# Kernel optimization log

Hardware: AMD Instinct MI355X
Metric: run time of the kernel (lower is better)

Reference implementation:

```python
import jax, jax.numpy as jnp
import numpy as np

H = 128
N = 20000
E = 640000

def _lin_params(key, fan_in, fan_out, bias=True):
    k1, k2 = jax.random.split(key)
    bound = 1.0 / np.sqrt(fan_in)
    W = jax.random.uniform(k1, (fan_in, fan_out), jnp.float32, -bound, bound)
    if bias:
        b = jax.random.uniform(k2, (fan_out,), jnp.float32, -bound, bound)
        return W, b
    return W, None

def setup_inputs() -> dict:
    key = jax.random.key(0)
    ks = jax.random.split(key, 10)
    h = jax.random.normal(ks[0], (N, H), jnp.float32)
    pos = jax.random.normal(ks[1], (N, 3), jnp.float32)
    edge_index = jax.random.randint(ks[2], (2, E), 0, N, jnp.int64)
    eW1, eb1 = _lin_params(ks[3], 2 * H + 1, H)
    eW2, eb2 = _lin_params(ks[4], H, H)
    cW1, cb1 = _lin_params(ks[5], H, H)
    cW2, _ = _lin_params(ks[6], H, 1, bias=False)
    nW1, nb1 = _lin_params(ks[7], 2 * H, H)
    nW2, nb2 = _lin_params(ks[8], H, H)
    return {"h": h, "pos": pos, "edge_index": edge_index,
            "eW1": eW1, "eb1": eb1, "eW2": eW2, "eb2": eb2,
            "cW1": cW1, "cb1": cb1, "cW2": cW2,
            "nW1": nW1, "nb1": nb1, "nW2": nW2, "nb2": nb2}

def reference(h, pos, edge_index, eW1, eb1, eW2, eb2, cW1, cb1, cW2, nW1, nb1, nW2, nb2):
    row, col = edge_index[0], edge_index[1]
    n = h.shape[0]
    # per-edge geometry
    coord_diff = pos[row] - pos[col]                      # [E, 3]
    sq_dists = jnp.sum(coord_diff ** 2, axis=-1, keepdims=True)  # [E, 1]
    # edge MLP: Linear -> SiLU -> Linear -> SiLU
    edge_inputs = jnp.concatenate([h[row], h[col], sq_dists], axis=-1)  # [E, 2H+1]
    m_ij = jax.nn.silu(jax.nn.silu(edge_inputs @ eW1 + eb1) @ eW2 + eb2)  # [E, H]
    # coord MLP: Linear -> SiLU -> Linear(no bias) -> scalar weight per edge
    coord_weights = jax.nn.silu(m_ij @ cW1 + cb1) @ cW2   # [E, 1]
    norm_coord_diff = coord_diff / jnp.sqrt(sq_dists + 1e-8)
    pos_updates_ij = norm_coord_diff * coord_weights      # [E, 3]
    # scatter-mean over target nodes (zero where a node has no edges)
    pos_sum = jax.ops.segment_sum(pos_updates_ij, row, num_segments=n)
    cnt = jax.ops.segment_sum(jnp.ones((row.shape[0], 1), h.dtype), row, num_segments=n)
    pos_out = pos + pos_sum / jnp.maximum(cnt, 1.0)
    # scatter-add messages, then node MLP with residual
    m_i = jax.ops.segment_sum(m_ij, row, num_segments=n)  # [N, H]
    node_inputs = jnp.concatenate([h, m_i], axis=-1)      # [N, 2H]
    h_out = h + (jax.nn.silu(node_inputs @ nW1 + nb1) @ nW2 + nb2)
    return h_out, pos_out
```

## Files before the change

### kernel.cpp

```cpp
#include <hip/hip_runtime.h>
#include <hip/hip_bf16.h>
#include <cstdint>

#define H 128
#define NNODES 20000
#define NEDGES 640000
#define TILE 64
#define SCAN_BLOCKS 20

typedef unsigned short ushort_t;
typedef __attribute__((ext_vector_type(8))) short short8;
typedef __attribute__((ext_vector_type(4))) float floatx4;
typedef __attribute__((ext_vector_type(2))) float floatx2;

__device__ __forceinline__ ushort_t f2bf(float f){
  uint32_t u = __builtin_bit_cast(uint32_t, f);
  u += 0x7fffu + ((u >> 16) & 1u);
  return (ushort_t)(u >> 16);
}
__device__ __forceinline__ float bf2f(ushort_t s){
  uint32_t u = ((uint32_t)s) << 16;
  return __builtin_bit_cast(float, u);
}
__device__ __forceinline__ uint32_t pk2bf(float lo, float hi){
  __hip_bfloat162 h2 = __float22bfloat162_rn(make_float2(lo, hi));
  uint32_t u;
  __builtin_memcpy(&u, &h2, 4);
  return u;
}
__device__ __forceinline__ floatx2 bfpair2(uint32_t u){
  floatx2 r;
  r.x = __builtin_bit_cast(float, u << 16);
  r.y = __builtin_bit_cast(float, u & 0xffff0000u);
  return r;
}
__device__ __forceinline__ float silu_f(float x){
  float e = __builtin_amdgcn_exp2f(-1.44269504089f * x);
  return x * __builtin_amdgcn_rcpf(1.f + e);
}

__global__ void setup_kernel(const float* __restrict__ eW1, const float* __restrict__ eW2,
                             const float* __restrict__ cW1, const float* __restrict__ nW1,
                             const float* __restrict__ nW2, const int* __restrict__ ei,
                             ushort_t* __restrict__ eW1t, ushort_t* __restrict__ eW2t,
                             ushort_t* __restrict__ cW1t, ushort_t* __restrict__ nW1t,
                             ushort_t* __restrict__ nW2t, uint32_t* __restrict__ w256b,
                             int* __restrict__ hist, float4* __restrict__ zbase){
  int idx = blockIdx.x * 256 + threadIdx.x;
  if (idx < 32768){
    int n = idx >> 8, k = idx & 255;
    eW1t[idx] = f2bf(eW1[k * H + n]);
  } else if (idx < 49152){
    int j = idx - 32768; int n = j >> 7, k = j & 127;
    eW2t[j] = f2bf(eW2[k * H + n]);
  } else if (idx < 65536){
    int j = idx - 49152; int n = j >> 7, k = j & 127;
    cW1t[j] = f2bf(cW1[k * H + n]);
  } else if (idx < 98304){
    int j = idx - 65536; int n = j >> 8, k = j & 255;
    nW1t[j] = f2bf(nW1[k * H + n]);
  } else if (idx < 114688){
    int j = idx - 98304; int n = j >> 7, k = j & 127;
    nW2t[j] = f2bf(nW2[k * H + n]);
  } else if (idx < 114752){
    int j = idx - 114688;
    w256b[j] = pk2bf(eW1[256 * H + 2*j], eW1[256 * H + 2*j + 1]);
  } else if (idx < 754752){
    int j = idx - 114752;
    atomicAdd(&hist[ei[j]], 1);
  } else {
    int j = idx - 754752;
    if (j < 655000) zbase[j] = make_float4(0.f, 0.f, 0.f, 0.f);
  }
}

__global__ void pq_kernel(const float* __restrict__ h, const ushort_t* __restrict__ eW1t,
                          const ushort_t* __restrict__ nW1t, const float* __restrict__ eb1,
                          ushort_t* __restrict__ Pb, ushort_t* __restrict__ Qb,
                          ushort_t* __restrict__ Rb){
  const int t = threadIdx.x;
  const int lane = t & 63, q = lane >> 4, ln = lane & 15;
  const int nb = (t >> 6) * 32;
  const int c0 = nb + 2 * ln;
  const int base = blockIdx.x * 64;

  floatx4 accP[4][2], accQ[4][2], accR[4][2];
  #pragma unroll
  for (int mt = 0; mt < 4; mt++)
    #pragma unroll
    for (int nt = 0; nt < 2; nt++){
      accP[mt][nt] = (floatx4)0.f; accQ[mt][nt] = (floatx4)0.f; accR[mt][nt] = (floatx4)0.f;
    }

  #pragma unroll
  for (int ks = 0; ks < 4; ks++){
    short8 a[4];
    #pragma unroll
    for (int mt = 0; mt < 4; mt++){
      int node = base + mt*16 + ln;
      if (node >= NNODES) node = NNODES - 1;
      const float* hp = h + (size_t)node * H + ks*32 + q*8;
      float4 v0 = *(const float4*)hp;
      float4 v1 = *(const float4*)(hp + 4);
      uint32_t tw[4];
      tw[0] = pk2bf(v0.x, v0.y); tw[1] = pk2bf(v0.z, v0.w);
      tw[2] = pk2bf(v1.x, v1.y); tw[3] = pk2bf(v1.z, v1.w);
      __builtin_memcpy(&a[mt], tw, 16);
    }
    short8 bP[2], bQ[2], bR[2];
    #pragma unroll
    for (int nt = 0; nt < 2; nt++){
      bP[nt] = *(const short8*)(eW1t + (size_t)(c0 + nt) * 256 + ks*32 + q*8);
      bQ[nt] = *(const short8*)(eW1t + (size_t)(c0 + nt) * 256 + 128 + ks*32 + q*8);
      bR[nt] = *(const short8*)(nW1t + (size_t)(c0 + nt) * 256 + ks*32 + q*8);
    }
    #pragma unroll
    for (int mt = 0; mt < 4; mt++)
      #pragma unroll
      for (int nt = 0; nt < 2; nt++){
        accP[mt][nt] = __builtin_amdgcn_mfma_f32_16x16x32_bf16(a[mt], bP[nt], accP[mt][nt], 0, 0, 0);
        accQ[mt][nt] = __builtin_amdgcn_mfma_f32_16x16x32_bf16(a[mt], bQ[nt], accQ[mt][nt], 0, 0, 0);
        accR[mt][nt] = __builtin_amdgcn_mfma_f32_16x16x32_bf16(a[mt], bR[nt], accR[mt][nt], 0, 0, 0);
      }
  }
  float2 e1 = *(const float2*)(eb1 + c0);
  #pragma unroll
  for (int mt = 0; mt < 4; mt++)
    #pragma unroll
    for (int r = 0; r < 4; r++){
      int node = base + mt*16 + q*4 + r;
      if (node < NNODES){
        *(uint32_t*)(Pb + (size_t)node * H + c0) = pk2bf(accP[mt][0][r] + e1.x, accP[mt][1][r] + e1.y);
        *(uint32_t*)(Qb + (size_t)node * H + c0) = pk2bf(accQ[mt][0][r], accQ[mt][1][r]);
        *(uint32_t*)(Rb + (size_t)node * H + c0) = pk2bf(accR[mt][0][r], accR[mt][1][r]);
      }
    }
}

__global__ void scanA_kernel(const int* __restrict__ hist, int* __restrict__ head,
                             int* __restrict__ totals){
  __shared__ int s[1024];
  const int t = threadIdx.x;
  const int idx = blockIdx.x * 1024 + t;
  int v = (idx < NNODES) ? hist[idx] : 0;
  s[t] = v;
  __syncthreads();
  for (int off = 1; off < 1024; off <<= 1){
    int tmp = (t >= off) ? s[t - off] : 0;
    __syncthreads();
    s[t] += tmp;
    __syncthreads();
  }
  if (idx < NNODES) head[idx] = s[t] - v;
  if (t == 1023) totals[blockIdx.x] = s[t];
}

__global__ void scanC_kernel(const int* __restrict__ totals, int* __restrict__ head){
  __shared__ int off_s;
  if (threadIdx.x == 0){
    int a = 0;
    for (int i = 0; i < (int)blockIdx.x; i++) a += totals[i];
    off_s = a;
  }
  __syncthreads();
  int idx = blockIdx.x * 1024 + threadIdx.x;
  if (idx < NNODES) head[idx] += off_s;
}

__global__ void scatter_kernel(const int* __restrict__ ei, int* __restrict__ head,
                               int2* __restrict__ spair){
  int idx = blockIdx.x * 256 + threadIdx.x;
  if (idx < NEDGES){
    int r = ei[idx], c = ei[NEDGES + idx];
    int p = atomicAdd(&head[r], 1);
    spair[p] = make_int2(r, c);
  }
}

__global__ __launch_bounds__(256, 8) void edge_kernel(
    const ushort_t* __restrict__ Pb, const ushort_t* __restrict__ Qb,
    const float* __restrict__ pos, const int2* __restrict__ spair,
    const uint32_t* __restrict__ w256b,
    const float* __restrict__ eb2, const float* __restrict__ cb1,
    const float* __restrict__ cW2,
    const ushort_t* __restrict__ eW2t, const ushort_t* __restrict__ cW1t,
    float* __restrict__ m_i, float* __restrict__ pos_sum)
{
  __shared__ __align__(16) ushort_t buf[TILE * 136];
  __shared__ int   row_l[TILE];
  __shared__ float sq_l[TILE];
  __shared__ float dx_l[TILE], dy_l[TILE], dz_l[TILE], w_l[TILE];

  const int t = threadIdx.x;
  const int base = blockIdx.x * TILE;
  const int lane = t & 63, q = lane >> 4, ln = lane & 15;
  const int nb = (t >> 6) * 32;
  const int c0 = nb + 2 * ln;

  {
    const int i = t >> 2, p = t & 3;
    int2 rc = spair[base + i];
    float ax = pos[rc.x*3+0] - pos[rc.y*3+0];
    float ay = pos[rc.x*3+1] - pos[rc.y*3+1];
    float az = pos[rc.x*3+2] - pos[rc.y*3+2];
    float sq = ax*ax + ay*ay + az*az;
    if (p == 0){
      row_l[i] = rc.x; sq_l[i] = sq;
      dx_l[i] = ax; dy_l[i] = ay; dz_l[i] = az;
      w_l[i] = 0.f;
    }
    floatx2 sq2; sq2.x = sq; sq2.y = sq;
    const uint4* Pp = (const uint4*)(Pb + (size_t)rc.x * H + p*32);
    const uint4* Qp = (const uint4*)(Qb + (size_t)rc.y * H + p*32);
    const uint4* Wp = (const uint4*)(w256b + p*16);
    ushort_t* dst = buf + i * 136 + p*32;
    #pragma unroll
    for (int j = 0; j < 4; j++){
      uint4 pv = Pp[j], qv = Qp[j], wv = Wp[j];
      uint32_t pvv[4] = {pv.x, pv.y, pv.z, pv.w};
      uint32_t qvv[4] = {qv.x, qv.y, qv.z, qv.w};
      uint32_t wvv[4] = {wv.x, wv.y, wv.z, wv.w};
      uint32_t outv[4];
      #pragma unroll
      for (int e = 0; e < 4; e++){
        floatx2 f = bfpair2(pvv[e]) + bfpair2(qvv[e]) + sq2 * bfpair2(wvv[e]);
        outv[e] = pk2bf(silu_f(f.x), silu_f(f.y));
      }
      uint4 out; __builtin_memcpy(&out, outv, 16);
      *(uint4*)(dst + j*8) = out;
    }
  }
  __syncthreads();

  floatx4 acc[4][2];

  #pragma unroll
  for (int mt = 0; mt < 4; mt++)
    #pragma unroll
    for (int nt = 0; nt < 2; nt++) acc[mt][nt] = (floatx4)0.f;
  #pragma unroll
  for (int ks = 0; ks < 4; ks++){
    short8 a[4], b[2];
    #pragma unroll
    for (int mt = 0; mt < 4; mt++)
      a[mt] = *(const short8*)(buf + (mt*16 + ln) * 136 + ks*32 + q*8);
    #pragma unroll
    for (int nt = 0; nt < 2; nt++)
      b[nt] = *(const short8*)(eW2t + (size_t)(c0 + nt) * 128 + ks*32 + q*8);
    #pragma unroll
    for (int mt = 0; mt < 4; mt++)
      #pragma unroll
      for (int nt = 0; nt < 2; nt++)
        acc[mt][nt] = __builtin_amdgcn_mfma_f32_16x16x32_bf16(a[mt], b[nt], acc[mt][nt], 0, 0, 0);
  }
  __syncthreads();
  {
    float2 e2 = *(const float2*)(eb2 + c0);
    #pragma unroll
    for (int mt = 0; mt < 4; mt++)
      #pragma unroll
      for (int r = 0; r < 4; r++){
        int m = mt*16 + q*4 + r;
        float f0 = silu_f(acc[mt][0][r] + e2.x);
        float f1 = silu_f(acc[mt][1][r] + e2.y);
        *(uint32_t*)(buf + m * 136 + c0) = pk2bf(f0, f1);
      }
  }
  __syncthreads();

  #pragma unroll
  for (int mt = 0; mt < 4; mt++)
    #pragma unroll
    for (int nt = 0; nt < 2; nt++) acc[mt][nt] = (floatx4)0.f;
  #pragma unroll
  for (int ks = 0; ks < 4; ks++){
    short8 a[4], b[2];
    #pragma unroll
    for (int mt = 0; mt < 4; mt++)
      a[mt] = *(const short8*)(buf + (mt*16 + ln) * 136 + ks*32 + q*8);
    #pragma unroll
    for (int nt = 0; nt < 2; nt++)
      b[nt] = *(const short8*)(cW1t + (size_t)(c0 + nt) * 128 + ks*32 + q*8);
    #pragma unroll
    for (int mt = 0; mt < 4; mt++)
      #pragma unroll
      for (int nt = 0; nt < 2; nt++)
        acc[mt][nt] = __builtin_amdgcn_mfma_f32_16x16x32_bf16(a[mt], b[nt], acc[mt][nt], 0, 0, 0);
  }
  {
    float2 c1 = *(const float2*)(cb1 + c0);
    float2 c2 = *(const float2*)(cW2 + c0);
    #pragma unroll
    for (int mt = 0; mt < 4; mt++)
      #pragma unroll
      for (int r = 0; r < 4; r++){
        float p = silu_f(acc[mt][0][r] + c1.x) * c2.x
                + silu_f(acc[mt][1][r] + c1.y) * c2.y;
        p += __shfl_xor(p, 1);
        p += __shfl_xor(p, 2);
        p += __shfl_xor(p, 4);
        p += __shfl_xor(p, 8);
        if (ln == 0) atomicAdd(&w_l[mt*16 + q*4 + r], p);
      }
  }
  __syncthreads();

  {
    int col = t & 127;
    int ms  = (t >> 7) * 32;
    float a0 = 0.f;
    int cur = row_l[ms];
    #pragma unroll 4
    for (int mm = 0; mm < 32; mm++){
      int m = ms + mm;
      int rr = row_l[m];
      float v = bf2f(buf[m * 136 + col]);
      if (rr != cur){
        unsafeAtomicAdd(&m_i[(size_t)cur * H + col], a0);
        a0 = 0.f; cur = rr;
      }
      a0 += v;
    }
    unsafeAtomicAdd(&m_i[(size_t)cur * H + col], a0);
  }
  if (t < 3){
    const float* src = (t == 0) ? dx_l : (t == 1) ? dy_l : dz_l;
    float accv = 0.f;
    int cur = row_l[0];
    for (int m = 0; m < TILE; m++){
      int rr = row_l[m];
      if (rr != cur){
        unsafeAtomicAdd(&pos_sum[cur*3 + t], accv);
        accv = 0.f; cur = rr;
      }
      float s = __builtin_amdgcn_rsqf(sq_l[m] + 1e-8f) * w_l[m];
      accv += src[m] * s;
    }
    unsafeAtomicAdd(&pos_sum[cur*3 + t], accv);
  }
}

__global__ __launch_bounds__(256, 8) void node_kernel(
    const float* __restrict__ h, const float* __restrict__ pos,
    const float* __restrict__ nb1, const float* __restrict__ nb2,
    const ushort_t* __restrict__ nW1t, const ushort_t* __restrict__ nW2t,
    const ushort_t* __restrict__ Rb,
    const float* __restrict__ m_i, const float* __restrict__ pos_sum,
    const int* __restrict__ hist,
    float* __restrict__ h_out, float* __restrict__ pos_out)
{
  __shared__ __align__(16) ushort_t bufT[32 * 136];
  const int t = threadIdx.x;
  const int base = blockIdx.x * 32;
  const int lane = t & 63, q = lane >> 4, ln = lane & 15;
  const int nb_ = (t >> 6) * 32;
  const int c0 = nb_ + 2 * ln;

  if (t < 32){
    int node = base + t;
    float c = fmaxf((float)hist[node], 1.f);
    float invc = __builtin_amdgcn_rcpf(c);
    pos_out[node*3+0] = pos[node*3+0] + pos_sum[node*3+0] * invc;
    pos_out[node*3+1] = pos[node*3+1] + pos_sum[node*3+1] * invc;
    pos_out[node*3+2] = pos[node*3+2] + pos_sum[node*3+2] * invc;
  }

  floatx4 acc[2][2];
  #pragma unroll
  for (int mt = 0; mt < 2; mt++)
    #pragma unroll
    for (int nt = 0; nt < 2; nt++) acc[mt][nt] = (floatx4)0.f;
  #pragma unroll
  for (int ks = 0; ks < 4; ks++){
    short8 a[2], b[2];
    #pragma unroll
    for (int mt = 0; mt < 2; mt++){
      const float* mp = m_i + (size_t)(base + mt*16 + ln) * H + ks*32 + q*8;
      float4 v0 = *(const float4*)mp;
      float4 v1 = *(const float4*)(mp + 4);
      uint32_t tw[4];
      tw[0] = pk2bf(v0.x, v0.y); tw[1] = pk2bf(v0.z, v0.w);
      tw[2] = pk2bf(v1.x, v1.y); tw[3] = pk2bf(v1.z, v1.w);
      __builtin_memcpy(&a[mt], tw, 16);
    }
    #pragma unroll
    for (int nt = 0; nt < 2; nt++)
      b[nt] = *(const short8*)(nW1t + (size_t)(c0 + nt) * 256 + 128 + ks*32 + q*8);
    #pragma unroll
    for (int mt = 0; mt < 2; mt++)
      #pragma unroll
      for (int nt = 0; nt < 2; nt++)
        acc[mt][nt] = __builtin_amdgcn_mfma_f32_16x16x32_bf16(a[mt], b[nt], acc[mt][nt], 0, 0, 0);
  }
  {
    float2 b1 = *(const float2*)(nb1 + c0);
    #pragma unroll
    for (int mt = 0; mt < 2; mt++)
      #pragma unroll
      for (int r = 0; r < 4; r++){
        int m = mt*16 + q*4 + r;
        int node = base + m;
        floatx2 rf = bfpair2(*(const uint32_t*)(Rb + (size_t)node * H + c0));
        float f0 = silu_f(acc[mt][0][r] + rf.x + b1.x);
        float f1 = silu_f(acc[mt][1][r] + rf.y + b1.y);
        *(uint32_t*)(bufT + m * 136 + c0) = pk2bf(f0, f1);
      }
  }
  __syncthreads();

  #pragma unroll
  for (int mt = 0; mt < 2; mt++)
    #pragma unroll
    for (int nt = 0; nt < 2; nt++) acc[mt][nt] = (floatx4)0.f;
  #pragma unroll
  for (int ks = 0; ks < 4; ks++){
    short8 a[2], b[2];
    #pragma unroll
    for (int mt = 0; mt < 2; mt++)
      a[mt] = *(const short8*)(bufT + (mt*16 + ln) * 136 + ks*32 + q*8);
    #pragma unroll
    for (int nt = 0; nt < 2; nt++)
      b[nt] = *(const short8*)(nW2t + (size_t)(c0 + nt) * 128 + ks*32 + q*8);
    #pragma unroll
    for (int mt = 0; mt < 2; mt++)
      #pragma unroll
      for (int nt = 0; nt < 2; nt++)
        acc[mt][nt] = __builtin_amdgcn_mfma_f32_16x16x32_bf16(a[mt], b[nt], acc[mt][nt], 0, 0, 0);
  }
  {
    float2 b2 = *(const float2*)(nb2 + c0);
    #pragma unroll
    for (int mt = 0; mt < 2; mt++)
      #pragma unroll
      for (int r = 0; r < 4; r++){
        int node = base + mt*16 + q*4 + r;
        const float2 hv = *(const float2*)(h + (size_t)node * H + c0);
        float2 o;
        o.x = hv.x + acc[mt][0][r] + b2.x;
        o.y = hv.y + acc[mt][1][r] + b2.y;
        *(float2*)(h_out + (size_t)node * H + c0) = o;
      }
  }
}

extern "C" void kernel_launch(void* const* d_in, const int* in_sizes, int n_in,
                              void* d_out, int out_size, void* d_ws, size_t ws_size,
                              hipStream_t stream){
  const float* h   = (const float*)d_in[0];
  const float* pos = (const float*)d_in[1];
  const int*   ei  = (const int*)d_in[2];
  const float* eW1 = (const float*)d_in[3];
  const float* eb1 = (const float*)d_in[4];
  const float* eW2 = (const float*)d_in[5];
  const float* eb2 = (const float*)d_in[6];
  const float* cW1 = (const float*)d_in[7];
  const float* cb1 = (const float*)d_in[8];
  const float* cW2 = (const float*)d_in[9];
  const float* nW1 = (const float*)d_in[10];
  const float* nb1 = (const float*)d_in[11];
  const float* nW2 = (const float*)d_in[12];
  const float* nb2 = (const float*)d_in[13];

  char* ws = (char*)d_ws;
  float*    m_i     = (float*)   (ws);
  float*    pos_sum = (float*)   (ws + 10240000);
  int*      hist    = (int*)     (ws + 10480000);
  int*      head    = (int*)     (ws + 10560000);
  int*      totals  = (int*)     (ws + 10640000);
  int2*     spair   = (int2*)    (ws + 10644096);
  ushort_t* Pb      = (ushort_t*)(ws + 15764096);
  ushort_t* eW1t    = (ushort_t*)(ws + 20884096);
  ushort_t* eW2t    = (ushort_t*)(ws + 20949632);
  ushort_t* cW1t    = (ushort_t*)(ws + 20982400);
  ushort_t* nW1t    = (ushort_t*)(ws + 21015168);
  ushort_t* nW2t    = (ushort_t*)(ws + 21080704);
  ushort_t* Qb      = (ushort_t*)(ws + 21113472);
  ushort_t* Rb      = (ushort_t*)(ws + 26233472);
  uint32_t* w256b   = (uint32_t*)(ws + 31353472);

  (void)hipMemsetAsync(hist, 0, 80000, stream);

  setup_kernel<<<5507, 256, 0, stream>>>(eW1, eW2, cW1, nW1, nW2, ei,
                                         eW1t, eW2t, cW1t, nW1t, nW2t, w256b, hist,
                                         (float4*)ws);
  pq_kernel<<<(NNODES + 63) / 64, 256, 0, stream>>>(h, eW1t, nW1t, eb1, Pb, Qb, Rb);
  scanA_kernel<<<SCAN_BLOCKS, 1024, 0, stream>>>(hist, head, totals);
  scanC_kernel<<<SCAN_BLOCKS, 1024, 0, stream>>>(totals, head);
  scatter_kernel<<<(NEDGES + 255) / 256, 256, 0, stream>>>(ei, head, spair);

  edge_kernel<<<NEDGES / TILE, 256, 0, stream>>>(Pb, Qb, pos, spair, w256b,
                                                 eb2, cb1, cW2,
                                                 eW2t, cW1t, m_i, pos_sum);

  float* h_out   = (float*)d_out;
  float* pos_out = h_out + (size_t)NNODES * H;
  node_kernel<<<NNODES / 32, 256, 0, stream>>>(h, pos, nb1, nb2,
                                               nW1t, nW2t, Rb, m_i, pos_sum,
                                               hist, h_out, pos_out);
}
```

Before: 361.3 us.

## Merge scan passes, fuse PQ GEMM with edge scatter, use memset for zeroing

New measurement: 367.5 us. Within noise of the previous version (+1.7%).

```diff
diff --git a/kernel.cpp b/kernel.cpp
--- a/kernel.cpp
+++ b/kernel.cpp
@@ -7,6 +7,7 @@
 #define NEDGES 640000
 #define TILE 64
 #define SCAN_BLOCKS 20
+#define PQ_BLOCKS 313
 
 typedef unsigned short ushort_t;
 typedef __attribute__((ext_vector_type(8))) short short8;
@@ -17,10 +18,6 @@
   uint32_t u = __builtin_bit_cast(uint32_t, f);
   u += 0x7fffu + ((u >> 16) & 1u);
   return (ushort_t)(u >> 16);
-}
-__device__ __forceinline__ float bf2f(ushort_t s){
-  uint32_t u = ((uint32_t)s) << 16;
-  return __builtin_bit_cast(float, u);
 }
 __device__ __forceinline__ uint32_t pk2bf(float lo, float hi){
   __hip_bfloat162 h2 = __float22bfloat162_rn(make_float2(lo, hi));
@@ -45,7 +42,7 @@
                              ushort_t* __restrict__ eW1t, ushort_t* __restrict__ eW2t,
                              ushort_t* __restrict__ cW1t, ushort_t* __restrict__ nW1t,
                              ushort_t* __restrict__ nW2t, uint32_t* __restrict__ w256b,
-                             int* __restrict__ hist, float4* __restrict__ zbase){
+                             int* __restrict__ hist){
   int idx = blockIdx.x * 256 + threadIdx.x;
   if (idx < 32768){
     int n = idx >> 8, k = idx & 255;
@@ -68,16 +65,59 @@
   } else if (idx < 754752){
     int j = idx - 114752;
     atomicAdd(&hist[ei[j]], 1);
-  } else {
-    int j = idx - 754752;
-    if (j < 655000) zbase[j] = make_float4(0.f, 0.f, 0.f, 0.f);
-  }
-}
-
-__global__ void pq_kernel(const float* __restrict__ h, const ushort_t* __restrict__ eW1t,
-                          const ushort_t* __restrict__ nW1t, const float* __restrict__ eb1,
-                          ushort_t* __restrict__ Pb, ushort_t* __restrict__ Qb,
-                          ushort_t* __restrict__ Rb){
+  }
+}
+
+__global__ void scan_kernel(const int* __restrict__ hist, int* __restrict__ head,
+                            int* __restrict__ flags, int* __restrict__ excl){
+  __shared__ int s[1024];
+  __shared__ int prev_s;
+  const int b = blockIdx.x, t = threadIdx.x;
+  const int idx = b * 1024 + t;
+  int v = (idx < NNODES) ? hist[idx] : 0;
+  s[t] = v;
+  __syncthreads();
+  for (int off = 1; off < 1024; off <<= 1){
+    int tmp = (t >= off) ? s[t - off] : 0;
+    __syncthreads();
+    s[t] += tmp;
+    __syncthreads();
+  }
+  if (t == 0){
+    int prev = 0;
+    if (b > 0){
+      while (atomicAdd(&flags[b], 0) == 0){}
+      __threadfence();
+      prev = atomicAdd(&excl[b], 0);
+    }
+    prev_s = prev;
+    if (b < SCAN_BLOCKS - 1){
+      atomicExch(&excl[b + 1], prev + s[1023]);
+      __threadfence();
+      atomicExch(&flags[b + 1], 1);
+    }
+  }
+  __syncthreads();
+  if (idx < NNODES) head[idx] = s[t] - v + prev_s;
+}
+
+__global__ void pqscatter_kernel(const float* __restrict__ h,
+                                 const ushort_t* __restrict__ eW1t,
+                                 const ushort_t* __restrict__ nW1t,
+                                 const float* __restrict__ eb1,
+                                 ushort_t* __restrict__ Pb, ushort_t* __restrict__ Qb,
+                                 ushort_t* __restrict__ Rb,
+                                 const int* __restrict__ ei, int* __restrict__ head,
+                                 int2* __restrict__ spair){
+  if (blockIdx.x >= PQ_BLOCKS){
+    int idx = (blockIdx.x - PQ_BLOCKS) * 256 + threadIdx.x;
+    if (idx < NEDGES){
+      int r = ei[idx], c = ei[NEDGES + idx];
+      int p = atomicAdd(&head[r], 1);
+      spair[p] = make_int2(r, c);
+    }
+    return;
+  }
   const int t = threadIdx.x;
   const int lane = t & 63, q = lane >> 4, ln = lane & 15;
   const int nb = (t >> 6) * 32;
@@ -135,46 +175,6 @@
         *(uint32_t*)(Rb + (size_t)node * H + c0) = pk2bf(accR[mt][0][r], accR[mt][1][r]);
       }
     }
-}
-
-__global__ void scanA_kernel(const int* __restrict__ hist, int* __restrict__ head,
-                             int* __restrict__ totals){
-  __shared__ int s[1024];
-  const int t = threadIdx.x;
-  const int idx = blockIdx.x * 1024 + t;
-  int v = (idx < NNODES) ? hist[idx] : 0;
-  s[t] = v;
-  __syncthreads();
-  for (int off = 1; off < 1024; off <<= 1){
-    int tmp = (t >= off) ? s[t - off] : 0;
-    __syncthreads();
-    s[t] += tmp;
-    __syncthreads();
-  }
-  if (idx < NNODES) head[idx] = s[t] - v;
-  if (t == 1023) totals[blockIdx.x] = s[t];
-}
-
-__global__ void scanC_kernel(const int* __restrict__ totals, int* __restrict__ head){
-  __shared__ int off_s;
-  if (threadIdx.x == 0){
-    int a = 0;
-    for (int i = 0; i < (int)blockIdx.x; i++) a += totals[i];
-    off_s = a;
-  }
-  __syncthreads();
-  int idx = blockIdx.x * 1024 + threadIdx.x;
-  if (idx < NNODES) head[idx] += off_s;
-}
-
-__global__ void scatter_kernel(const int* __restrict__ ei, int* __restrict__ head,
-                               int2* __restrict__ spair){
-  int idx = blockIdx.x * 256 + threadIdx.x;
-  if (idx < NEDGES){
-    int r = ei[idx], c = ei[NEDGES + idx];
-    int p = atomicAdd(&head[r], 1);
-    spair[p] = make_int2(r, c);
-  }
 }
 
 __global__ __launch_bounds__(256, 8) void edge_kernel(
@@ -305,38 +305,41 @@
   }
   __syncthreads();
 
-  {
-    int col = t & 127;
-    int ms  = (t >> 7) * 32;
-    float a0 = 0.f;
+  if (t < 128){
+    int cp = (t & 63) * 2;
+    int ms = (t >> 6) * 32;
+    float a0 = 0.f, a1 = 0.f;
     int cur = row_l[ms];
     #pragma unroll 4
     for (int mm = 0; mm < 32; mm++){
       int m = ms + mm;
       int rr = row_l[m];
-      float v = bf2f(buf[m * 136 + col]);
+      uint32_t v = *(const uint32_t*)(buf + m * 136 + cp);
       if (rr != cur){
-        unsafeAtomicAdd(&m_i[(size_t)cur * H + col], a0);
-        a0 = 0.f; cur = rr;
-      }
-      a0 += v;
-    }
-    unsafeAtomicAdd(&m_i[(size_t)cur * H + col], a0);
-  }
-  if (t < 3){
-    const float* src = (t == 0) ? dx_l : (t == 1) ? dy_l : dz_l;
+        unsafeAtomicAdd(&m_i[(size_t)cur * H + cp],     a0);
+        unsafeAtomicAdd(&m_i[(size_t)cur * H + cp + 1], a1);
+        a0 = 0.f; a1 = 0.f; cur = rr;
+      }
+      floatx2 f = bfpair2(v);
+      a0 += f.x; a1 += f.y;
+    }
+    unsafeAtomicAdd(&m_i[(size_t)cur * H + cp],     a0);
+    unsafeAtomicAdd(&m_i[(size_t)cur * H + cp + 1], a1);
+  } else if (t < 131){
+    const int d = t - 128;
+    const float* src = (d == 0) ? dx_l : (d == 1) ? dy_l : dz_l;
     float accv = 0.f;
     int cur = row_l[0];
     for (int m = 0; m < TILE; m++){
       int rr = row_l[m];
       if (rr != cur){
-        unsafeAtomicAdd(&pos_sum[cur*3 + t], accv);
+        unsafeAtomicAdd(&pos_sum[cur*3 + d], accv);
         accv = 0.f; cur = rr;
       }
       float s = __builtin_amdgcn_rsqf(sq_l[m] + 1e-8f) * w_l[m];
       accv += src[m] * s;
     }
-    unsafeAtomicAdd(&pos_sum[cur*3 + t], accv);
+    unsafeAtomicAdd(&pos_sum[cur*3 + d], accv);
   }
 }
 
@@ -465,8 +468,9 @@
   float*    m_i     = (float*)   (ws);
   float*    pos_sum = (float*)   (ws + 10240000);
   int*      hist    = (int*)     (ws + 10480000);
-  int*      head    = (int*)     (ws + 10560000);
-  int*      totals  = (int*)     (ws + 10640000);
+  int*      flags   = (int*)     (ws + 10560000);
+  int*      excl    = (int*)     (ws + 10560128);
+  int*      head    = (int*)     (ws + 10560256);
   int2*     spair   = (int2*)    (ws + 10644096);
   ushort_t* Pb      = (ushort_t*)(ws + 15764096);
   ushort_t* eW1t    = (ushort_t*)(ws + 20884096);
@@ -478,15 +482,13 @@
   ushort_t* Rb      = (ushort_t*)(ws + 26233472);
   uint32_t* w256b   = (uint32_t*)(ws + 31353472);
 
-  (void)hipMemsetAsync(hist, 0, 80000, stream);
-
-  setup_kernel<<<5507, 256, 0, stream>>>(eW1, eW2, cW1, nW1, nW2, ei,
-                                         eW1t, eW2t, cW1t, nW1t, nW2t, w256b, hist,
-                                         (float4*)ws);
-  pq_kernel<<<(NNODES + 63) / 64, 256, 0, stream>>>(h, eW1t, nW1t, eb1, Pb, Qb, Rb);
-  scanA_kernel<<<SCAN_BLOCKS, 1024, 0, stream>>>(hist, head, totals);
-  scanC_kernel<<<SCAN_BLOCKS, 1024, 0, stream>>>(totals, head);
-  scatter_kernel<<<(NEDGES + 255) / 256, 256, 0, stream>>>(ei, head, spair);
+  (void)hipMemsetAsync(ws, 0, 10560256, stream);
+
+  setup_kernel<<<2949, 256, 0, stream>>>(eW1, eW2, cW1, nW1, nW2, ei,
+                                         eW1t, eW2t, cW1t, nW1t, nW2t, w256b, hist);
+  scan_kernel<<<SCAN_BLOCKS, 1024, 0, stream>>>(hist, head, flags, excl);
+  pqscatter_kernel<<<PQ_BLOCKS + (NEDGES + 255) / 256, 256, 0, stream>>>(
+      h, eW1t, nW1t, eb1, Pb, Qb, Rb, ei, head, spair);
 
   edge_kernel<<<NEDGES / TILE, 256, 0, stream>>>(Pb, Qb, pos, spair, w256b,
                                                  eb2, cb1, cW2,
```
